# Kernel tuning notes

Measured on AMD Instinct MI355X. Metric: run time of the kernel, lower is better.

Reference implementation:

```python
import jax, jax.numpy as jnp
import numpy as np

B, NQ, NK, C = 8, 1024, 1024, 1024
H, DK, DV = 16, 64, 64


def setup_inputs() -> dict:
    key = jax.random.key(0)
    ks = jax.random.split(key, 10)
    queries = jax.random.normal(ks[0], (B, NQ, C), dtype=jnp.float32)
    keys_ = jax.random.normal(ks[1], (B, NK, C), dtype=jnp.float32)
    values = jax.random.normal(ks[2], (B, NK, C), dtype=jnp.float32)
    attention_mask = jax.random.randint(ks[3], (B, H, NQ, NK), 0, 2).astype(jnp.bool_)
    attention_weights = jax.random.uniform(ks[4], (B, H, NQ, NK), dtype=jnp.float32)
    std = 0.001  # init.normal_(m.weight, std=0.001), bias=0
    Wq = jax.random.normal(ks[5], (C, H * DK), dtype=jnp.float32) * std
    Wk = jax.random.normal(ks[6], (C, H * DK), dtype=jnp.float32) * std
    Wv = jax.random.normal(ks[7], (C, H * DV), dtype=jnp.float32) * std
    Wo = jax.random.normal(ks[8], (H * DV, C), dtype=jnp.float32) * std
    bq = jnp.zeros((H * DK,), jnp.float32)
    bk = jnp.zeros((H * DK,), jnp.float32)
    bv = jnp.zeros((H * DV,), jnp.float32)
    bo = jnp.zeros((C,), jnp.float32)
    return {"queries": queries, "keys": keys_, "values": values,
            "attention_mask": attention_mask, "attention_weights": attention_weights,
            "Wq": Wq, "bq": bq, "Wk": Wk, "bk": bk, "Wv": Wv, "bv": bv,
            "Wo": Wo, "bo": bo}


def reference(queries, keys, values, attention_mask, attention_weights,
              Wq, bq, Wk, bk, Wv, bv, Wo, bo):
    bs, nq, _ = queries.shape
    nk = keys.shape[1]
    # projections -> (b, h, n, d)
    q = (queries @ Wq + bq).reshape(bs, nq, H, DK).transpose(0, 2, 1, 3)
    k = (keys @ Wk + bk).reshape(bs, nk, H, DK).transpose(0, 2, 1, 3)
    v = (values @ Wv + bv).reshape(bs, nk, H, DV).transpose(0, 2, 1, 3)
    att = jnp.einsum('bhqd,bhkd->bhqk', q, k) / np.sqrt(DK).astype(np.float32)
    att = att * attention_weights
    att = jnp.where(attention_mask, -jnp.inf, att)
    att = jax.nn.softmax(att, axis=-1)
    # dropout is identity in eval mode
    out = jnp.einsum('bhqk,bhkd->bhqd', att, v)
    out = out.transpose(0, 2, 1, 3).reshape(bs, nq, H * DV)
    return out @ Wo + bo
```

## Files before the change

### kernel.cpp

```cpp
#include <hip/hip_runtime.h>
#include <hip/hip_bf16.h>

using short8 = __attribute__((ext_vector_type(8))) short;
using f32x4  = __attribute__((ext_vector_type(4))) float;

__device__ __forceinline__ unsigned short f2bf(float f) {
    union { float f; unsigned u; } x; x.f = f;
    unsigned r = x.u + 0x7FFFu + ((x.u >> 16) & 1u);
    return (unsigned short)(r >> 16);
}

__device__ __forceinline__ void gload_lds16(const void* g, void* l) {
    __builtin_amdgcn_global_load_lds(
        (const __attribute__((address_space(1))) unsigned int*)g,
        (__attribute__((address_space(3))) unsigned int*)l, 16, 0, 0);
}

__global__ void detect_mask_kernel(const unsigned int* __restrict__ m, int* __restrict__ flag) {
    if (threadIdx.x == 0) *flag = 0;
    __syncthreads();
    unsigned v = m[threadIdx.x];
    if (v > 1u) {
        atomicOr(flag, 1);
        if (v != 0x3F800000u) atomicOr(flag, 2);
    }
}

__global__ __launch_bounds__(256) void maskpack_kernel(
    const void* __restrict__ mask, const int* __restrict__ flag,
    unsigned long long* __restrict__ Mb, int nwords)
{
    const int l = threadIdx.x & 63;
    const int gwave = (int)((blockIdx.x * 256 + threadIdx.x) >> 6);
    const int nw = (int)((gridDim.x * 256) >> 6);
    const bool bytem = ((*flag) & 2) != 0;
    const unsigned char* m8 = (const unsigned char*)mask;
    const unsigned int* m32 = (const unsigned int*)mask;
    for (int w0 = gwave * 4; w0 < nwords; w0 += nw * 4) {
        unsigned v[4];
#pragma unroll
        for (int u = 0; u < 4; u++) {
            size_t e = (size_t)(w0 + u) * 64 + l;
            v[u] = bytem ? (unsigned)m8[e] : m32[e];
        }
#pragma unroll
        for (int u = 0; u < 4; u++) {
            unsigned long long b = __ballot(v[u] != 0u);
            if (l == 0) Mb[w0 + u] = b;
        }
    }
}

__global__ __launch_bounds__(256) void wconv_kernel(
    const float* __restrict__ W0, const float* __restrict__ W1,
    const float* __restrict__ W2, const float* __restrict__ W3,
    unsigned short* __restrict__ Wt)
{
    const int z = blockIdx.z;
    const float* W = (z == 0) ? W0 : ((z == 1) ? W1 : ((z == 2) ? W2 : W3));
    unsigned short* O = Wt + (size_t)z * 1024 * 1024;
    __shared__ float tile[64][68];
    const int t = threadIdx.x;
    const int k0 = blockIdx.x * 64, n0 = blockIdx.y * 64;
    const int rr = t >> 4, cc = t & 15;
#pragma unroll
    for (int i = 0; i < 4; i++) {
        int row = rr + i * 16;
        float4 v = *reinterpret_cast<const float4*>(W + (size_t)(k0 + row) * 1024 + n0 + cc * 4);
        *reinterpret_cast<float4*>(&tile[row][cc * 4]) = v;
    }
    __syncthreads();
#pragma unroll
    for (int i = 0; i < 4; i++) {
        int rn = rr + i * 16;
        ushort4 ov;
        ov.x = f2bf(tile[cc * 4 + 0][rn]);
        ov.y = f2bf(tile[cc * 4 + 1][rn]);
        ov.z = f2bf(tile[cc * 4 + 2][rn]);
        ov.w = f2bf(tile[cc * 4 + 3][rn]);
        *reinterpret_cast<ushort4*>(O + (size_t)(n0 + rn) * 1024 + k0 + cc * 4) = ov;
    }
}

__global__ __launch_bounds__(256) void aconv_kernel(
    const float* __restrict__ Aq, const float* __restrict__ Ak, const float* __restrict__ Av,
    unsigned short* __restrict__ Out)
{
    const int z = blockIdx.y;
    const float* A = (z == 0) ? Aq : ((z == 1) ? Ak : Av);
    unsigned short* O = Out + (size_t)z * 8192 * 1024;
    size_t i = ((size_t)blockIdx.x * 256 + threadIdx.x) * 8;
    float4 v0 = *reinterpret_cast<const float4*>(A + i);
    float4 v1 = *reinterpret_cast<const float4*>(A + i + 4);
    short8 o;
    o[0] = (short)f2bf(v0.x); o[1] = (short)f2bf(v0.y);
    o[2] = (short)f2bf(v0.z); o[3] = (short)f2bf(v0.w);
    o[4] = (short)f2bf(v1.x); o[5] = (short)f2bf(v1.y);
    o[6] = (short)f2bf(v1.z); o[7] = (short)f2bf(v1.w);
    *reinterpret_cast<short8*>(O + i) = o;
}

#define GEMM_CORE(A_PTR, W_PTR)                                                             \
    __shared__ unsigned short Ab[2][4096];                                                  \
    __shared__ unsigned short Bb[2][4096];                                                  \
    const int tid = threadIdx.x, w = tid >> 6, l = tid & 63, l16 = l & 15, g = l >> 4;      \
    const int wr = w >> 1, wc = w & 1;                                                      \
    const int row0 = blockIdx.x * 128, col0 = blockIdx.y * 128;                             \
    const int offs = tid * 16;                                                              \
    const char* gA0 = (const char*)(A_PTR) + (size_t)(row0 + (offs >> 6)) * 2048 + (offs & 63);          \
    const char* gA1 = (const char*)(A_PTR) + (size_t)(row0 + ((offs + 4096) >> 6)) * 2048 + (offs & 63); \
    const char* gB0 = (const char*)(W_PTR) + (size_t)(col0 + (offs >> 6)) * 2048 + (offs & 63);          \
    const char* gB1 = (const char*)(W_PTR) + (size_t)(col0 + ((offs + 4096) >> 6)) * 2048 + (offs & 63); \
    char* ldsAw0 = (char*)Ab[0] + w * 1024; char* ldsAw0b = (char*)Ab[0] + 4096 + w * 1024; \
    char* ldsAw1 = (char*)Ab[1] + w * 1024; char* ldsAw1b = (char*)Ab[1] + 4096 + w * 1024; \
    char* ldsBw0 = (char*)Bb[0] + w * 1024; char* ldsBw0b = (char*)Bb[0] + 4096 + w * 1024; \
    char* ldsBw1 = (char*)Bb[1] + w * 1024; char* ldsBw1b = (char*)Bb[1] + 4096 + w * 1024; \
    const char* rdA = (char*)Ab[0] + (wr * 64 + l16) * 64 + g * 16;    \
    const char* rdB = (char*)Bb[0] + (wc * 64 + l16) * 64 + g * 16;                         \
    f32x4 acc[4][4];                                                                        \
    _Pragma("unroll")                                                                       \
    for (int i = 0; i < 4; i++)                                                             \
        _Pragma("unroll")                                                                   \
        for (int j = 0; j < 4; j++) acc[i][j] = (f32x4){0.f, 0.f, 0.f, 0.f};                \
    gload_lds16(gA0, ldsAw0); gload_lds16(gA1, ldsAw0b);                                    \
    gload_lds16(gB0, ldsBw0); gload_lds16(gB1, ldsBw0b);                                    \
    asm volatile("s_waitcnt vmcnt(0)" ::: "memory");                                        \
    __builtin_amdgcn_s_barrier();                                                           \
    for (int kt = 0; kt < 32; kt++) {                                                       \
        const int buf = kt & 1;                                                             \
        if (kt < 31) {                                                                      \
            const int ko = (kt + 1) * 64;                                                   \
            if (buf == 0) {                                                                 \
                gload_lds16(gA0 + ko, ldsAw1); gload_lds16(gA1 + ko, ldsAw1b);              \
                gload_lds16(gB0 + ko, ldsBw1); gload_lds16(gB1 + ko, ldsBw1b);              \
            } else {                                                                        \
                gload_lds16(gA0 + ko, ldsAw0); gload_lds16(gA1 + ko, ldsAw0b);              \
                gload_lds16(gB0 + ko, ldsBw0); gload_lds16(gB1 + ko, ldsBw0b);              \
            }                                                                               \
        }                                                                                   \
        short8 af[4], bfm[4];                                                               \
        _Pragma("unroll")                                                                   \
        for (int fr = 0; fr < 4; fr++)                                                      \
            af[fr] = *reinterpret_cast<const short8*>(rdA + buf * 8192 + fr * 1024);        \
        _Pragma("unroll")                                                                   \
        for (int fc = 0; fc < 4; fc++)                                                      \
            bfm[fc] = *reinterpret_cast<const short8*>(rdB + buf * 8192 + fc * 1024);       \
        _Pragma("unroll")                                                                   \
        for (int fr = 0; fr < 4; fr++)                                                      \
            _Pragma("unroll")                                                               \
            for (int fc = 0; fc < 4; fc++)                                                  \
                acc[fr][fc] = __builtin_amdgcn_mfma_f32_16x16x32_bf16(af[fr], bfm[fc], acc[fr][fc], 0, 0, 0); \
        asm volatile("s_waitcnt vmcnt(0)" ::: "memory");                                    \
        __builtin_amdgcn_s_barrier();                                                       \
    }

__global__ __launch_bounds__(256, 3) void gemm_proj_kernel(
    const unsigned short* __restrict__ Abf,
    const unsigned short* __restrict__ Wt,
    const float* __restrict__ bq, const float* __restrict__ bk, const float* __restrict__ bv,
    unsigned short* __restrict__ Out)
{
    const int z = blockIdx.z;
    const unsigned short* A = Abf + (size_t)z * 8192 * 1024;
    const unsigned short* Wz = Wt + (size_t)z * 1024 * 1024;
    const float* bias = (z == 0) ? bq : ((z == 1) ? bk : bv);
    unsigned short* Oz = Out + (size_t)z * 8 * 16 * 1024 * 64;

    GEMM_CORE(A, Wz)

#pragma unroll
    for (int fr = 0; fr < 4; fr++)
#pragma unroll
        for (int fc = 0; fc < 4; fc++)
#pragma unroll
            for (int r = 0; r < 4; r++) {
                int row = row0 + wr * 64 + fr * 16 + g * 4 + r;
                int col = col0 + wc * 64 + fc * 16 + l16;
                float val = acc[fr][fc][r] + bias[col];
                int bb = row >> 10, n = row & 1023;
                int h = col >> 6, d = col & 63;
                Oz[(((size_t)(bb * 16 + h)) * 1024 + n) * 64 + d] = f2bf(val);
            }
}

__global__ __launch_bounds__(256, 3) void gemm_out_kernel(
    const unsigned short* __restrict__ Ain,
    const unsigned short* __restrict__ Wto,
    const float* __restrict__ bo,
    float* __restrict__ Out)
{
    GEMM_CORE(Ain, Wto)

#pragma unroll
    for (int fr = 0; fr < 4; fr++)
#pragma unroll
        for (int fc = 0; fc < 4; fc++)
#pragma unroll
            for (int r = 0; r < 4; r++) {
                int row = row0 + wr * 64 + fr * 16 + g * 4 + r;
                int col = col0 + wc * 64 + fc * 16 + l16;
                Out[(size_t)row * 1024 + col] = acc[fr][fc][r] + bo[col];
            }
}

__global__ __launch_bounds__(256) void proj_f32_kernel(
    const float* __restrict__ Aq, const float* __restrict__ Ak, const float* __restrict__ Av,
    const unsigned short* __restrict__ Wt,
    const float* __restrict__ bq, const float* __restrict__ bk, const float* __restrict__ bv,
    unsigned short* __restrict__ Out)
{
    const int z = blockIdx.z;
    const float* A = (z == 0) ? Aq : ((z == 1) ? Ak : Av);
    const float* bias = (z == 0) ? bq : ((z == 1) ? bk : bv);
    const unsigned short* Wz = Wt + (size_t)z * 1024 * 1024;
    unsigned short* Oz = Out + (size_t)z * 8 * 16 * 1024 * 64;

    const int tid = threadIdx.x;
    const int w = tid >> 6, l = tid & 63;
    const int l16 = l & 15, g = l >> 4;
    const int rbase = blockIdx.x * 128 + w * 32;
    const int cbase = blockIdx.y * 64;

    f32x4 acc[2][4];
#pragma unroll
    for (int i = 0; i < 2; i++)
#pragma unroll
        for (int j = 0; j < 4; j++) acc[i][j] = (f32x4){0.f, 0.f, 0.f, 0.f};

#pragma unroll 2
    for (int k0 = 0; k0 < 1024; k0 += 32) {
        short8 a[2];
#pragma unroll
        for (int rf = 0; rf < 2; rf++) {
            const float* ap = A + (size_t)(rbase + rf * 16 + l16) * 1024 + k0 + g * 8;
            float4 v0 = *reinterpret_cast<const float4*>(ap);
            float4 v1 = *reinterpret_cast<const float4*>(ap + 4);
            short8 av;
            av[0] = (short)f2bf(v0.x); av[1] = (short)f2bf(v0.y);
            av[2] = (short)f2bf(v0.z); av[3] = (short)f2bf(v0.w);
            av[4] = (short)f2bf(v1.x); av[5] = (short)f2bf(v1.y);
            av[6] = (short)f2bf(v1.z); av[7] = (short)f2bf(v1.w);
            a[rf] = av;
        }
        short8 bfr[4];
#pragma unroll
        for (int cf = 0; cf < 4; cf++)
            bfr[cf] = *reinterpret_cast<const short8*>(Wz + (size_t)(cbase + cf * 16 + l16) * 1024 + k0 + g * 8);
#pragma unroll
        for (int rf = 0; rf < 2; rf++)
#pragma unroll
            for (int cf = 0; cf < 4; cf++)
                acc[rf][cf] = __builtin_amdgcn_mfma_f32_16x16x32_bf16(a[rf], bfr[cf], acc[rf][cf], 0, 0, 0);
    }

#pragma unroll
    for (int rf = 0; rf < 2; rf++)
#pragma unroll
        for (int cf = 0; cf < 4; cf++)
#pragma unroll
            for (int r = 0; r < 4; r++) {
                int row = rbase + rf * 16 + g * 4 + r;
                int col = cbase + cf * 16 + l16;
                float val = acc[rf][cf][r] + bias[col];
                int bb = row >> 10, n = row & 1023;
                int h = col >> 6, d = col & 63;
                Oz[(((size_t)(bb * 16 + h)) * 1024 + n) * 64 + d] = f2bf(val);
            }
}

__global__ __launch_bounds__(256) void vtrans_kernel(
    const unsigned short* __restrict__ Vs, unsigned short* __restrict__ Vt)
{
    const int bh = blockIdx.y;
    const int k0 = blockIdx.x * 64;
    const unsigned short* In = Vs + (size_t)bh * 1024 * 64;
    unsigned short* O = Vt + (size_t)bh * 64 * 1024;
    __shared__ unsigned short tile[64][72];
    const int t = threadIdx.x;
    {
        const int row = t >> 3;
        const int c8 = (t & 7) * 8;
#pragma unroll
        for (int i = 0; i < 2; i++) {
            int r = row + i * 32;
            short8 v = *reinterpret_cast<const short8*>(In + (size_t)(k0 + r) * 64 + c8);
            *reinterpret_cast<short8*>(&tile[r][c8]) = v;
        }
    }
    __syncthreads();
    {
        const int rd = t >> 4, c4 = (t & 15) * 4;
#pragma unroll
        for (int i = 0; i < 4; i++) {
            int d = rd + i * 16;
            ushort4 ov;
            ov.x = tile[c4 + 0][d];
            ov.y = tile[c4 + 1][d];
            ov.z = tile[c4 + 2][d];
            ov.w = tile[c4 + 3][d];
            *reinterpret_cast<ushort4*>(O + (size_t)d * 1024 + k0 + c4) = ov;
        }
    }
}

__global__ __launch_bounds__(512, 4) void attn_kernel(
    const unsigned short* __restrict__ Qs,
    const unsigned short* __restrict__ Ks,
    const unsigned short* __restrict__ Vt,
    const float* __restrict__ attw,
    const unsigned long long* __restrict__ Mb,
    unsigned short* __restrict__ AO)
{
    __shared__ char smem[51200];

    const int bid = blockIdx.x;
    const int xj = bid & 7, xp = bid >> 3;
    const int qt = xp & 7;
    const int gbh = (xp >> 3) * 8 + xj;
    const int h = gbh & 15, b = gbh >> 4;
    const int bh = b * 16 + h;

    const int tid = threadIdx.x, w = tid >> 6, l = tid & 63, l16 = l & 15, g = l >> 4;
    const int myq = qt * 128 + w * 16 + l16;

    const unsigned short* Qbh = Qs + (size_t)bh * 65536;
    const char* Kb = (const char*)(Ks + (size_t)bh * 65536);
    const char* Vb = (const char*)(Vt + (size_t)bh * 65536);
    const float* wrow = attw + ((size_t)bh * 1024 + myq) * 1024;
    const unsigned long long* mrow = Mb + ((size_t)bh * 1024 + myq) * 16;

    const int srow = w * 8 + (l >> 3);
    const int sinn = ((l & 7) * 16) ^ (((l >> 3) & 7) << 4);
    const char* gK = Kb + (size_t)srow * 128 + sinn;
    const char* gV = Vb + (size_t)srow * 2048 + sinn;
    char* ldsK0w = smem + 0     + w * 1024;
    char* ldsK1w = smem + 8192  + w * 1024;
    char* ldsV0w = smem + 16384 + w * 1024;
    char* ldsV1w = smem + 24576 + w * 1024;

    const int rswz = (l16 & 7) << 4;
    char* kaddrA = smem + l16 * 128 + ((g * 16) ^ rswz);
    char* kaddrB = smem + l16 * 128 + ((64 + g * 16) ^ rswz);
    char* pw = smem + 32768 + w * 2304 + l16 * 144 + g * 8;
    char* pr = smem + 32768 + w * 2304 + l16 * 144 + g * 16;

    short8 qf0 = *reinterpret_cast<const short8*>(Qbh + (size_t)myq * 64 + g * 8);
    short8 qf1 = *reinterpret_cast<const short8*>(Qbh + (size_t)myq * 64 + 32 + g * 8);

    float4 wvA[4], wvB[4];
    unsigned long long mbA, mbB;

    gload_lds16(gK, ldsK0w);
    gload_lds16(gV, ldsV0w);
    gK += 8192; gV += 128;
#pragma unroll
    for (int cf = 0; cf < 4; cf++)
        wvA[cf] = *reinterpret_cast<const float4*>(wrow + cf * 16 + g * 4);
    mbA = mrow[0];
#pragma unroll
    for (int cf = 0; cf < 4; cf++)
        wvB[cf] = *reinterpret_cast<const float4*>(wrow + 64 + cf * 16 + g * 4);
    mbB = mrow[1];
    asm volatile("s_waitcnt vmcnt(10)" ::: "memory");
    __builtin_amdgcn_s_barrier();
    __builtin_amdgcn_sched_barrier(0);

    f32x4 accO[4];
#pragma unroll
    for (int j = 0; j < 4; j++) accO[j] = (f32x4){0.f, 0.f, 0.f, 0.f};
    float den = 0.f;

#define ATTN_ITER(KT, BUF, WVC, MBC)                                                        \
    {                                                                                       \
        if ((KT) < 15) {                                                                    \
            gload_lds16(gK, (BUF) ? ldsK0w : ldsK1w);                                       \
            gload_lds16(gV, (BUF) ? ldsV0w : ldsV1w);                                       \
        }                                                                                   \
        gK += 8192; gV += 128;                                                              \
        _Pragma("unroll")                                                                   \
        for (int cf = 0; cf < 4; cf++) {                                                    \
            short8 k0 = *reinterpret_cast<const short8*>(kaddrA + (BUF) * 8192 + cf * 2048);\
            short8 k1 = *reinterpret_cast<const short8*>(kaddrB + (BUF) * 8192 + cf * 2048);\
            f32x4 s = (f32x4){0.f, 0.f, 0.f, 0.f};                                          \
            s = __builtin_amdgcn_mfma_f32_16x16x32_bf16(k0, qf0, s, 0, 0, 0);               \
            s = __builtin_amdgcn_mfma_f32_16x16x32_bf16(k1, qf1, s, 0, 0, 0);               \
            unsigned mn = (unsigned)((MBC) >> (cf * 16 + g * 4)) & 0xFu;                    \
            float p0 = (mn & 1u) ? 0.f : __expf(s[0] * 0.125f * (WVC)[cf].x);               \
            float p1 = (mn & 2u) ? 0.f : __expf(s[1] * 0.125f * (WVC)[cf].y);               \
            float p2 = (mn & 4u) ? 0.f : __expf(s[2] * 0.125f * (WVC)[cf].z);               \
            float p3 = (mn & 8u) ? 0.f : __expf(s[3] * 0.125f * (WVC)[cf].w);               \
            den += p0 + p1 + p2 + p3;                                                       \
            ushort4 pwv;                                                                    \
            pwv.x = f2bf(p0); pwv.y = f2bf(p1); pwv.z = f2bf(p2); pwv.w = f2bf(p3);         \
            *reinterpret_cast<ushort4*>(pw + cf * 32) = pwv;                                \
        }                                                                                   \
        {                                                                                   \
            const int ktn = ((KT) + 2) & 15;                                                \
            _Pragma("unroll")                                                               \
            for (int cf = 0; cf < 4; cf++)                                                  \
                (WVC)[cf] = *reinterpret_cast<const float4*>(wrow + ktn * 64 + cf * 16 + g * 4); \
            (MBC) = mrow[ktn];                                                              \
        }                                                                                   \
        {                                                                                   \
            short8 pf0 = *reinterpret_cast<const short8*>(pr);                              \
            short8 pf1 = *reinterpret_cast<const short8*>(pr + 64);                         \
            _Pragma("unroll")                                                               \
            for (int cf = 0; cf < 4; cf++) {                                                \
                short8 v0 = *reinterpret_cast<const short8*>(kaddrA + 16384 + (BUF) * 8192 + cf * 2048); \
                short8 v1 = *reinterpret_cast<const short8*>(kaddrB + 16384 + (BUF) * 8192 + cf * 2048); \
                accO[cf] = __builtin_amdgcn_mfma_f32_16x16x32_bf16(pf0, v0, accO[cf], 0, 0, 0); \
                accO[cf] = __builtin_amdgcn_mfma_f32_16x16x32_bf16(pf1, v1, accO[cf], 0, 0, 0); \
            }                                                                               \
        }                                                                                   \
        asm volatile("s_waitcnt vmcnt(5)" ::: "memory");                                    \
        __builtin_amdgcn_s_barrier();                                                       \
        __builtin_amdgcn_sched_barrier(0);                                                  \
    }

    for (int kt2 = 0; kt2 < 16; kt2 += 2) {
        ATTN_ITER(kt2, 0, wvA, mbA);
        ATTN_ITER(kt2 + 1, 1, wvB, mbB);
    }
#undef ATTN_ITER

    den += __shfl_xor(den, 16);
    den += __shfl_xor(den, 32);

#pragma unroll
    for (int r = 0; r < 4; r++) {
        float dr = __shfl(den, g * 4 + r);
        float inv = 1.0f / dr;
#pragma unroll
        for (int cf = 0; cf < 4; cf++) {
            int qrow = qt * 128 + w * 16 + g * 4 + r;
            int col = h * 64 + cf * 16 + l16;
            AO[((size_t)b * 1024 + qrow) * 1024 + col] = f2bf(accO[cf][r] * inv);
        }
    }
}

extern "C" void kernel_launch(void* const* d_in, const int* in_sizes, int n_in,
                              void* d_out, int out_size, void* d_ws, size_t ws_size,
                              hipStream_t stream)
{
    const float* queries = (const float*)d_in[0];
    const float* keys    = (const float*)d_in[1];
    const float* values  = (const float*)d_in[2];
    const void*  mask    = d_in[3];
    const float* attw    = (const float*)d_in[4];
    const float* Wq = (const float*)d_in[5];
    const float* bq = (const float*)d_in[6];
    const float* Wk = (const float*)d_in[7];
    const float* bk = (const float*)d_in[8];
    const float* Wv = (const float*)d_in[9];
    const float* bv = (const float*)d_in[10];
    const float* Wo = (const float*)d_in[11];
    const float* bo = (const float*)d_in[12];

    char* ws = (char*)d_ws;
    int* flag = (int*)ws;
    unsigned short* base = (unsigned short*)(ws + 256);
    const size_t M8 = (size_t)8 * 1024 * 1024;
    unsigned short* Qs  = base;
    unsigned short* Ksb = base + M8;
    unsigned short* Vs  = base + 2 * M8;
    unsigned short* Vtb = base + 3 * M8;
    unsigned short* AO  = base + 4 * M8;
    unsigned short* Wt  = base + 5 * M8;
    unsigned short* Abf = base + 5 * M8 + 4 * 1024 * 1024;
    unsigned long long* Mb = (unsigned long long*)Vs;
    const size_t need_abf = 256 + (5 * M8 + 4 * 1024 * 1024 + 3 * M8) * sizeof(unsigned short);
    const bool useAbf = ws_size >= need_abf;

    detect_mask_kernel<<<1, 256, 0, stream>>>((const unsigned int*)mask, flag);
    wconv_kernel<<<dim3(16, 16, 4), 256, 0, stream>>>(Wq, Wk, Wv, Wo, Wt);
    if (useAbf) {
        aconv_kernel<<<dim3(4096, 3), 256, 0, stream>>>(queries, keys, values, Abf);
        gemm_proj_kernel<<<dim3(64, 8, 3), 256, 0, stream>>>(Abf, Wt, bq, bk, bv, Qs);
    } else {
        proj_f32_kernel<<<dim3(64, 16, 3), 256, 0, stream>>>(queries, keys, values, Wt, bq, bk, bv, Qs);
    }
    vtrans_kernel<<<dim3(16, 128), 256, 0, stream>>>(Vs, Vtb);
    maskpack_kernel<<<dim3(2048), 256, 0, stream>>>(mask, flag, Mb, 2 * 1024 * 1024);
    attn_kernel<<<dim3(1024), 512, 0, stream>>>(Qs, Ksb, Vtb, attw, Mb, AO);
    gemm_out_kernel<<<dim3(64, 8), 256, 0, stream>>>(AO, Wt + (size_t)3 * 1024 * 1024, bo, (float*)d_out);
}
```

Measured before the change: 419.1 us.

## Triple-buffer GEMM and attention K loads with deeper prefetch pipelines

```diff
diff --git a/kernel.cpp b/kernel.cpp
--- a/kernel.cpp
+++ b/kernel.cpp
@@ -100,9 +100,49 @@
     *reinterpret_cast<short8*>(O + i) = o;
 }
 
+#define GEMM_IT(KT, RB, SB, DOST, WN)                                                       \
+    {                                                                                       \
+        if (DOST) {                                                                         \
+            const int ko = ((KT) + 2) * 64;                                                 \
+            gload_lds16(gA0 + ko, lA0_##SB); gload_lds16(gA1 + ko, lA1_##SB);               \
+            gload_lds16(gB0 + ko, lB0_##SB); gload_lds16(gB1 + ko, lB1_##SB);               \
+        }                                                                                   \
+        short8 af[4], bfm[4];                                                               \
+        _Pragma("unroll")                                                                   \
+        for (int fr = 0; fr < 4; fr++)                                                      \
+            af[fr] = *reinterpret_cast<const short8*>(rdA + (RB) * 8192 + fr * 1024);       \
+        _Pragma("unroll")                                                                   \
+        for (int fc = 0; fc < 4; fc++)                                                      \
+            bfm[fc] = *reinterpret_cast<const short8*>(rdB + (RB) * 8192 + fc * 1024);      \
+        _Pragma("unroll")                                                                   \
+        for (int fr = 0; fr < 4; fr++)                                                      \
+            _Pragma("unroll")                                                               \
+            for (int fc = 0; fc < 4; fc++)                                                  \
+                acc[fr][fc] = __builtin_amdgcn_mfma_f32_16x16x32_bf16(af[fr], bfm[fc], acc[fr][fc], 0, 0, 0); \
+        asm volatile("s_waitcnt vmcnt(" #WN ")" ::: "memory");                              \
+        __builtin_amdgcn_s_barrier();                                                       \
+        __builtin_amdgcn_sched_barrier(0);                                                  \
+    }
+
+#define GEMM_IT_LAST(RB)                                                                    \
+    {                                                                                       \
+        short8 af[4], bfm[4];                                                               \
+        _Pragma("unroll")                                                                   \
+        for (int fr = 0; fr < 4; fr++)                                                      \
+            af[fr] = *reinterpret_cast<const short8*>(rdA + (RB) * 8192 + fr * 1024);       \
+        _Pragma("unroll")                                                                   \
+        for (int fc = 0; fc < 4; fc++)                                                      \
+            bfm[fc] = *reinterpret_cast<const short8*>(rdB + (RB) * 8192 + fc * 1024);      \
+        _Pragma("unroll")                                                                   \
+        for (int fr = 0; fr < 4; fr++)                                                      \
+            _Pragma("unroll")                                                               \
+            for (int fc = 0; fc < 4; fc++)                                                  \
+                acc[fr][fc] = __builtin_amdgcn_mfma_f32_16x16x32_bf16(af[fr], bfm[fc], acc[fr][fc], 0, 0, 0); \
+    }
+
 #define GEMM_CORE(A_PTR, W_PTR)                                                             \
-    __shared__ unsigned short Ab[2][4096];                                                  \
-    __shared__ unsigned short Bb[2][4096];                                                  \
+    __shared__ unsigned short Ab[3][4096];                                                  \
+    __shared__ unsigned short Bb[3][4096];                                                  \
     const int tid = threadIdx.x, w = tid >> 6, l = tid & 63, l16 = l & 15, g = l >> 4;      \
     const int wr = w >> 1, wc = w & 1;                                                      \
     const int row0 = blockIdx.x * 128, col0 = blockIdx.y * 128;                             \
@@ -111,48 +151,33 @@
     const char* gA1 = (const char*)(A_PTR) + (size_t)(row0 + ((offs + 4096) >> 6)) * 2048 + (offs & 63); \
     const char* gB0 = (const char*)(W_PTR) + (size_t)(col0 + (offs >> 6)) * 2048 + (offs & 63);          \
     const char* gB1 = (const char*)(W_PTR) + (size_t)(col0 + ((offs + 4096) >> 6)) * 2048 + (offs & 63); \
-    char* ldsAw0 = (char*)Ab[0] + w * 1024; char* ldsAw0b = (char*)Ab[0] + 4096 + w * 1024; \
-    char* ldsAw1 = (char*)Ab[1] + w * 1024; char* ldsAw1b = (char*)Ab[1] + 4096 + w * 1024; \
-    char* ldsBw0 = (char*)Bb[0] + w * 1024; char* ldsBw0b = (char*)Bb[0] + 4096 + w * 1024; \
-    char* ldsBw1 = (char*)Bb[1] + w * 1024; char* ldsBw1b = (char*)Bb[1] + 4096 + w * 1024; \
-    const char* rdA = (char*)Ab[0] + (wr * 64 + l16) * 64 + g * 16;    \
+    char* lA0_0 = (char*)Ab[0] + w * 1024; char* lA1_0 = (char*)Ab[0] + 4096 + w * 1024;    \
+    char* lA0_1 = (char*)Ab[1] + w * 1024; char* lA1_1 = (char*)Ab[1] + 4096 + w * 1024;    \
+    char* lA0_2 = (char*)Ab[2] + w * 1024; char* lA1_2 = (char*)Ab[2] + 4096 + w * 1024;    \
+    char* lB0_0 = (char*)Bb[0] + w * 1024; char* lB1_0 = (char*)Bb[0] + 4096 + w * 1024;    \
+    char* lB0_1 = (char*)Bb[1] + w * 1024; char* lB1_1 = (char*)Bb[1] + 4096 + w * 1024;    \
+    char* lB0_2 = (char*)Bb[2] + w * 1024; char* lB1_2 = (char*)Bb[2] + 4096 + w * 1024;    \
+    const char* rdA = (char*)Ab[0] + (wr * 64 + l16) * 64 + g * 16;                         \
     const char* rdB = (char*)Bb[0] + (wc * 64 + l16) * 64 + g * 16;                         \
     f32x4 acc[4][4];                                                                        \
     _Pragma("unroll")                                                                       \
     for (int i = 0; i < 4; i++)                                                             \
         _Pragma("unroll")                                                                   \
         for (int j = 0; j < 4; j++) acc[i][j] = (f32x4){0.f, 0.f, 0.f, 0.f};                \
-    gload_lds16(gA0, ldsAw0); gload_lds16(gA1, ldsAw0b);                                    \
-    gload_lds16(gB0, ldsBw0); gload_lds16(gB1, ldsBw0b);                                    \
-    asm volatile("s_waitcnt vmcnt(0)" ::: "memory");                                        \
+    gload_lds16(gA0, lA0_0); gload_lds16(gA1, lA1_0);                                       \
+    gload_lds16(gB0, lB0_0); gload_lds16(gB1, lB1_0);                                       \
+    gload_lds16(gA0 + 64, lA0_1); gload_lds16(gA1 + 64, lA1_1);                             \
+    gload_lds16(gB0 + 64, lB0_1); gload_lds16(gB1 + 64, lB1_1);                             \
+    asm volatile("s_waitcnt vmcnt(4)" ::: "memory");                                        \
     __builtin_amdgcn_s_barrier();                                                           \
-    for (int kt = 0; kt < 32; kt++) {                                                       \
-        const int buf = kt & 1;                                                             \
-        if (kt < 31) {                                                                      \
-            const int ko = (kt + 1) * 64;                                                   \
-            if (buf == 0) {                                                                 \
-                gload_lds16(gA0 + ko, ldsAw1); gload_lds16(gA1 + ko, ldsAw1b);              \
-                gload_lds16(gB0 + ko, ldsBw1); gload_lds16(gB1 + ko, ldsBw1b);              \
-            } else {                                                                        \
-                gload_lds16(gA0 + ko, ldsAw0); gload_lds16(gA1 + ko, ldsAw0b);              \
-                gload_lds16(gB0 + ko, ldsBw0); gload_lds16(gB1 + ko, ldsBw0b);              \
-            }                                                                               \
-        }                                                                                   \
-        short8 af[4], bfm[4];                                                               \
-        _Pragma("unroll")                                                                   \
-        for (int fr = 0; fr < 4; fr++)                                                      \
-            af[fr] = *reinterpret_cast<const short8*>(rdA + buf * 8192 + fr * 1024);        \
-        _Pragma("unroll")                                                                   \
-        for (int fc = 0; fc < 4; fc++)                                                      \
-            bfm[fc] = *reinterpret_cast<const short8*>(rdB + buf * 8192 + fc * 1024);       \
-        _Pragma("unroll")                                                                   \
-        for (int fr = 0; fr < 4; fr++)                                                      \
-            _Pragma("unroll")                                                               \
-            for (int fc = 0; fc < 4; fc++)                                                  \
-                acc[fr][fc] = __builtin_amdgcn_mfma_f32_16x16x32_bf16(af[fr], bfm[fc], acc[fr][fc], 0, 0, 0); \
-        asm volatile("s_waitcnt vmcnt(0)" ::: "memory");                                    \
-        __builtin_amdgcn_s_barrier();                                                       \
-    }
+    __builtin_amdgcn_sched_barrier(0);                                                      \
+    for (int kt0 = 0; kt0 < 30; kt0 += 3) {                                                 \
+        GEMM_IT(kt0 + 0, 0, 2, 1, 4)                                                        \
+        GEMM_IT(kt0 + 1, 1, 0, 1, 4)                                                        \
+        GEMM_IT(kt0 + 2, 2, 1, 1, 4)                                                        \
+    }                                                                                       \
+    GEMM_IT(30, 0, 0, 0, 0)                                                                 \
+    GEMM_IT_LAST(1)
 
 __global__ __launch_bounds__(256, 3) void gemm_proj_kernel(
     const unsigned short* __restrict__ Abf,
@@ -311,7 +336,7 @@
     const unsigned long long* __restrict__ Mb,
     unsigned short* __restrict__ AO)
 {
-    __shared__ char smem[51200];
+    __shared__ __align__(16) char smem[59392];
 
     const int bid = blockIdx.x;
     const int xj = bid & 7, xp = bid >> 3;
@@ -333,16 +358,17 @@
     const int sinn = ((l & 7) * 16) ^ (((l >> 3) & 7) << 4);
     const char* gK = Kb + (size_t)srow * 128 + sinn;
     const char* gV = Vb + (size_t)srow * 2048 + sinn;
-    char* ldsK0w = smem + 0     + w * 1024;
-    char* ldsK1w = smem + 8192  + w * 1024;
-    char* ldsV0w = smem + 16384 + w * 1024;
-    char* ldsV1w = smem + 24576 + w * 1024;
+    char* lK_0 = smem + 0     + w * 1024;
+    char* lK_1 = smem + 8192  + w * 1024;
+    char* lK_2 = smem + 16384 + w * 1024;
+    char* lV_0 = smem + 24576 + w * 1024;
+    char* lV_1 = smem + 32768 + w * 1024;
 
     const int rswz = (l16 & 7) << 4;
-    char* kaddrA = smem + l16 * 128 + ((g * 16) ^ rswz);
-    char* kaddrB = smem + l16 * 128 + ((64 + g * 16) ^ rswz);
-    char* pw = smem + 32768 + w * 2304 + l16 * 144 + g * 8;
-    char* pr = smem + 32768 + w * 2304 + l16 * 144 + g * 16;
+    const int krdA = l16 * 128 + ((g * 16) ^ rswz);
+    const int krdB = l16 * 128 + ((64 + g * 16) ^ rswz);
+    char* pw = smem + 40960 + w * 2304 + l16 * 144 + g * 8;
+    char* pr = smem + 40960 + w * 2304 + l16 * 144 + g * 16;
 
     short8 qf0 = *reinterpret_cast<const short8*>(Qbh + (size_t)myq * 64 + g * 8);
     short8 qf1 = *reinterpret_cast<const short8*>(Qbh + (size_t)myq * 64 + 32 + g * 8);
@@ -350,9 +376,9 @@
     float4 wvA[4], wvB[4];
     unsigned long long mbA, mbB;
 
-    gload_lds16(gK, ldsK0w);
-    gload_lds16(gV, ldsV0w);
-    gK += 8192; gV += 128;
+    gload_lds16(gK, lK_0);
+    gload_lds16(gK + 8192, lK_1);
+    gload_lds16(gV, lV_0);
 #pragma unroll
     for (int cf = 0; cf < 4; cf++)
         wvA[cf] = *reinterpret_cast<const float4*>(wrow + cf * 16 + g * 4);
@@ -361,7 +387,7 @@
     for (int cf = 0; cf < 4; cf++)
         wvB[cf] = *reinterpret_cast<const float4*>(wrow + 64 + cf * 16 + g * 4);
     mbB = mrow[1];
-    asm volatile("s_waitcnt vmcnt(10)" ::: "memory");
+    asm volatile("s_waitcnt vmcnt(12)" ::: "memory");
     __builtin_amdgcn_s_barrier();
     __builtin_amdgcn_sched_barrier(0);
 
@@ -370,17 +396,14 @@
     for (int j = 0; j < 4; j++) accO[j] = (f32x4){0.f, 0.f, 0.f, 0.f};
     float den = 0.f;
 
-#define ATTN_ITER(KT, BUF, WVC, MBC)                                                        \
+#define AITER(KT, KB, VB, KSB, VSB, WVC, MBC, W1N)                                          \
     {                                                                                       \
-        if ((KT) < 15) {                                                                    \
-            gload_lds16(gK, (BUF) ? ldsK0w : ldsK1w);                                       \
-            gload_lds16(gV, (BUF) ? ldsV0w : ldsV1w);                                       \
-        }                                                                                   \
-        gK += 8192; gV += 128;                                                              \
+        if ((KT) <= 14) gload_lds16(gV + ((KT) + 1) * 128, lV_##VSB);                       \
+        if ((KT) <= 13) gload_lds16(gK + ((KT) + 2) * 8192, lK_##KSB);                      \
         _Pragma("unroll")                                                                   \
         for (int cf = 0; cf < 4; cf++) {                                                    \
-            short8 k0 = *reinterpret_cast<const short8*>(kaddrA + (BUF) * 8192 + cf * 2048);\
-            short8 k1 = *reinterpret_cast<const short8*>(kaddrB + (BUF) * 8192 + cf * 2048);\
+            short8 k0 = *reinterpret_cast<const short8*>(smem + (KB) * 8192 + krdA + cf * 2048); \
+            short8 k1 = *reinterpret_cast<const short8*>(smem + (KB) * 8192 + krdB + cf * 2048); \
             f32x4 s = (f32x4){0.f, 0.f, 0.f, 0.f};                                          \
             s = __builtin_amdgcn_mfma_f32_16x16x32_bf16(k0, qf0, s, 0, 0, 0);               \
             s = __builtin_amdgcn_mfma_f32_16x16x32_bf16(k1, qf1, s, 0, 0, 0);               \
@@ -394,34 +417,51 @@
             pwv.x = f2bf(p0); pwv.y = f2bf(p1); pwv.z = f2bf(p2); pwv.w = f2bf(p3);         \
             *reinterpret_cast<ushort4*>(pw + cf * 32) = pwv;                                \
         }                                                                                   \
-        {                                                                                   \
-            const int ktn = ((KT) + 2) & 15;                                                \
+        if ((KT) <= 13) {                                                                   \
             _Pragma("unroll")                                                               \
             for (int cf = 0; cf < 4; cf++)                                                  \
-                (WVC)[cf] = *reinterpret_cast<const float4*>(wrow + ktn * 64 + cf * 16 + g * 4); \
-            (MBC) = mrow[ktn];                                                              \
+                (WVC)[cf] = *reinterpret_cast<const float4*>(wrow + ((KT) + 2) * 64 + cf * 16 + g * 4); \
+            (MBC) = mrow[(KT) + 2];                                                         \
         }                                                                                   \
+        asm volatile("s_waitcnt vmcnt(" #W1N ")" ::: "memory");                             \
+        __builtin_amdgcn_s_barrier();                                                       \
+        __builtin_amdgcn_sched_barrier(0);                                                  \
         {                                                                                   \
             short8 pf0 = *reinterpret_cast<const short8*>(pr);                              \
             short8 pf1 = *reinterpret_cast<const short8*>(pr + 64);                         \
             _Pragma("unroll")                                                               \
             for (int cf = 0; cf < 4; cf++) {                                                \
-                short8 v0 = *reinterpret_cast<const short8*>(kaddrA + 16384 + (BUF) * 8192 + cf * 2048); \
-                short8 v1 = *reinterpret_cast<const short8*>(kaddrB + 16384 + (BUF) * 8192 + cf * 2048); \
+                short8 v0 = *reinterpret_cast<const short8*>(smem + 24576 + (VB) * 8192 + krdA + cf * 2048); \
+                short8 v1 = *reinterpret_cast<const short8*>(smem + 24576 + (VB) * 8192 + krdB + cf * 2048); \
                 accO[cf] = __builtin_amdgcn_mfma_f32_16x16x32_bf16(pf0, v0, accO[cf], 0, 0, 0); \
                 accO[cf] = __builtin_amdgcn_mfma_f32_16x16x32_bf16(pf1, v1, accO[cf], 0, 0, 0); \
             }                                                                               \
         }                                                                                   \
-        asm volatile("s_waitcnt vmcnt(5)" ::: "memory");                                    \
-        __builtin_amdgcn_s_barrier();                                                       \
-        __builtin_amdgcn_sched_barrier(0);                                                  \
-    }
-
-    for (int kt2 = 0; kt2 < 16; kt2 += 2) {
-        ATTN_ITER(kt2, 0, wvA, mbA);
-        ATTN_ITER(kt2 + 1, 1, wvB, mbB);
-    }
-#undef ATTN_ITER
+    }
+
+#define AITER_W2(W2N)                                                                       \
+    asm volatile("s_waitcnt vmcnt(" #W2N ")" ::: "memory");                                 \
+    __builtin_amdgcn_s_barrier();                                                           \
+    __builtin_amdgcn_sched_barrier(0);
+
+    AITER(0,  0, 0, 2, 1, wvA, mbA, 13) AITER_W2(12)
+    AITER(1,  1, 1, 0, 0, wvB, mbB, 13) AITER_W2(12)
+    AITER(2,  2, 0, 1, 1, wvA, mbA, 13) AITER_W2(12)
+    AITER(3,  0, 1, 2, 0, wvB, mbB, 13) AITER_W2(12)
+    AITER(4,  1, 0, 0, 1, wvA, mbA, 13) AITER_W2(12)
+    AITER(5,  2, 1, 1, 0, wvB, mbB, 13) AITER_W2(12)
+    AITER(6,  0, 0, 2, 1, wvA, mbA, 13) AITER_W2(12)
+    AITER(7,  1, 1, 0, 0, wvB, mbB, 13) AITER_W2(12)
+    AITER(8,  2, 0, 1, 1, wvA, mbA, 13) AITER_W2(12)
+    AITER(9,  0, 1, 2, 0, wvB, mbB, 13) AITER_W2(12)
+    AITER(10, 1, 0, 0, 1, wvA, mbA, 13) AITER_W2(12)
+    AITER(11, 2, 1, 1, 0, wvB, mbB, 13) AITER_W2(12)
+    AITER(12, 0, 0, 2, 1, wvA, mbA, 13) AITER_W2(12)
+    AITER(13, 1, 1, 0, 0, wvB, mbB, 13) AITER_W2(12)
+    AITER(14, 2, 0, 0, 1, wvA, mbA, 7)  AITER_W2(6)
+    AITER(15, 0, 1, 0, 0, wvB, mbB, 0)
+#undef AITER
+#undef AITER_W2
 
     den += __shfl_xor(den, 16);
     den += __shfl_xor(den, 32);
```

Result: slower. 607.0 us (+44.8%).
